# Performance work log

Hardware: AMD Instinct MI355X
Metric: run time of the kernel (lower is better)

The kernel has to match this reference:

```python
import jax, jax.numpy as jnp
import numpy as np


def setup_inputs() -> dict:
    key = jax.random.key(0)
    ks = jax.random.split(key, 8)
    bs, slen, d = 16, 2048, 1024
    scale = 1.0 / np.sqrt(d)
    return {
        "query": jax.random.normal(ks[0], (bs, d), jnp.float32),
        "states": jax.random.normal(ks[1], (bs, slen, d), jnp.float32),
        "Wq": jax.random.normal(ks[2], (d, d), jnp.float32) * scale,
        "bq": jax.random.normal(ks[3], (d,), jnp.float32) * 0.01,
        "Wk": jax.random.normal(ks[4], (d, d), jnp.float32) * scale,
        "bk": jax.random.normal(ks[5], (d,), jnp.float32) * 0.01,
        "We": jax.random.normal(ks[6], (2 * d,), jnp.float32) * scale,
        "be": jax.random.normal(ks[7], (1,), jnp.float32) * 0.01,
    }


def reference(query, states, Wq, bq, Wk, bk, We, be):
    d = Wq.shape[1]
    # q: (bs, d); k: (bs, slen, d)
    q = jax.nn.relu(query @ Wq + bq)
    k = jax.nn.relu(jnp.einsum("bsv,vd->bsd", states, Wk) + bk)
    # tanh(cat(q, k)) @ We == tanh(q) @ We[:d] + tanh(k) @ We[d:]
    # (avoids materializing the repeated/concatenated (bs, slen, 2d) tensor)
    We_q, We_k = We[:d], We[d:]
    energy = (jnp.tanh(q) @ We_q)[:, None] + jnp.einsum("bsd,d->bs", jnp.tanh(k), We_k) + be[0]
    attn_weights = jax.nn.softmax(energy, axis=1)  # (bs, slen)
    attn = jnp.einsum("bs,bsd->bd", attn_weights, states)  # weighted sum of values
    return attn_weights, attn
```

## Files before the change

kernel.cpp:

```cpp
#include <hip/hip_runtime.h>
#include <hip/hip_bf16.h>

#define D 1024
#define SLEN 2048
#define BS 16
#define MROWS (BS*SLEN)

typedef __attribute__((ext_vector_type(8))) short short8;
typedef __attribute__((ext_vector_type(4))) float f32x4;

__device__ __forceinline__ short f2bf(float f) {
  __hip_bfloat16 h = __float2bfloat16(f);
  return __builtin_bit_cast(short, h);
}

__device__ __forceinline__ float4 ntload4(const float* p) {
  f32x4 v = __builtin_nontemporal_load((const f32x4*)p);
  float4 r; r.x = v.x; r.y = v.y; r.z = v.z; r.w = v.w; return r;
}

__global__ __launch_bounds__(256) void wk_prep(const float* __restrict__ Wk,
                                               short* __restrict__ WkT) {
  const int g = blockIdx.x;
  const int t = threadIdx.x;
#pragma unroll
  for (int it = 0; it < 4; ++it) {
    const int n = it*256 + t;
    short8 p;
#pragma unroll
    for (int j = 0; j < 8; ++j)
      p[j] = f2bf(Wk[(size_t)(g*8 + j)*D + n]);
    *(short8*)(WkT + ((size_t)g*D + n)*8) = p;
  }
}

__global__ __launch_bounds__(512, 2) void energy_gemm(
    const float* __restrict__ states, const short* __restrict__ WkT,
    const float* __restrict__ bk, const float* __restrict__ We,
    float* __restrict__ eraw, float* __restrict__ attn)
{
  __shared__ short Al[64 * 129 * 8];

  const int tid  = threadIdx.x;
  const int w    = tid >> 6;
  const int lane = tid & 63;
  const int quad = lane >> 4;
  const int l16  = lane & 15;
  const int m0   = blockIdx.x * 64;

  if (blockIdx.x < BS && tid < 256) {
    f32x4 z = {0.f, 0.f, 0.f, 0.f};
    *(f32x4*)(attn + (size_t)blockIdx.x*D + tid*4) = z;
  }

  {
    const int row = tid >> 3;
    const int u0  = tid & 7;
    const float* Ag = states + (size_t)(m0 + row)*D;
#pragma unroll
    for (int i = 0; i < 16; ++i) {
      const int u = u0 + i*8;
      float4 x0 = ntload4(Ag + u*8);
      float4 x1 = ntload4(Ag + u*8 + 4);
      short8 p;
      p[0]=f2bf(x0.x); p[1]=f2bf(x0.y); p[2]=f2bf(x0.z); p[3]=f2bf(x0.w);
      p[4]=f2bf(x1.x); p[5]=f2bf(x1.y); p[6]=f2bf(x1.z); p[7]=f2bf(x1.w);
      *(short8*)(Al + ((size_t)row*129 + u)*8) = p;
    }
  }
  __syncthreads();

  const short* bbase = WkT + ((size_t)quad*D + w*128 + l16)*8;
  const short* abase = Al + ((size_t)l16*129 + quad)*8;

  float esum[16];
#pragma unroll
  for (int q = 0; q < 16; ++q) esum[q] = 0.f;

#define LOADB3(ks, slot)                                                 \
  {                                                                      \
    const short* bp = bpass + (size_t)(ks)*32768;                        \
    _Pragma("unroll")                                                    \
    for (int ni = 0; ni < 4; ++ni)                                       \
      fb[slot][ni] = *(const short8*)(bp + ni*128);                      \
  }

#define LOADA(ks, buf)                                                   \
  {                                                                      \
    _Pragma("unroll")                                                    \
    for (int mi = 0; mi < 4; ++mi)                                       \
      buf[mi] = *(const short8*)(abase + mi*16512 + (ks)*32);            \
  }

#define MFMAS16(fa, slot)                                                \
  {                                                                      \
    __builtin_amdgcn_s_setprio(1);                                       \
    _Pragma("unroll")                                                    \
    for (int mi = 0; mi < 4; ++mi)                                       \
      _Pragma("unroll")                                                  \
      for (int ni = 0; ni < 4; ++ni)                                     \
        acc[mi][ni] = __builtin_amdgcn_mfma_f32_16x16x32_bf16(           \
            fa[mi], fb[slot][ni], acc[mi][ni], 0, 0, 0);                 \
    __builtin_amdgcn_s_setprio(0);                                       \
  }

#pragma unroll
  for (int np = 0; np < 2; ++np) {
    const short* bpass = bbase + np*512;

    f32x4 acc[4][4];
#pragma unroll
    for (int mi = 0; mi < 4; ++mi)
#pragma unroll
      for (int ni = 0; ni < 4; ++ni)
        acc[mi][ni] = (f32x4){0.f, 0.f, 0.f, 0.f};

    short8 fb[3][4];
    short8 fa0[4], fa1[4];
    LOADB3(0, 0); LOADB3(1, 1); LOADB3(2, 2);
    LOADA(0, fa0);
#pragma unroll
    for (int kk = 0; kk < 16; ++kk) {
      LOADA(2*kk + 1, fa1);
      MFMAS16(fa0, (2*kk) % 3);
      if (2*kk + 3 < 32) LOADB3(2*kk + 3, (2*kk) % 3);
      if (kk < 15) LOADA(2*kk + 2, fa0);
      MFMAS16(fa1, (2*kk + 1) % 3);
      if (2*kk + 4 < 32) LOADB3(2*kk + 4, (2*kk + 1) % 3);
    }

#pragma unroll
    for (int ni = 0; ni < 4; ++ni) {
      const int n = w*128 + np*64 + ni*16 + l16;
      const float bkv = bk[n];
      const float wev = We[D + n];
#pragma unroll
      for (int mi = 0; mi < 4; ++mi)
#pragma unroll
        for (int r = 0; r < 4; ++r) {
          float x = acc[mi][ni][r] + bkv;
          x = fmaxf(x, 0.f);
          float ex = __expf(2.f * x);
          float th = 1.f - 2.f/(ex + 1.f);
          esum[mi*4 + r] += th * wev;
        }
    }
  }

#pragma unroll
  for (int dd = 1; dd < 16; dd <<= 1)
#pragma unroll
    for (int q = 0; q < 16; ++q)
      esum[q] += __shfl_xor(esum[q], dd, 64);

  __syncthreads();
  float* red = (float*)Al;
  if (l16 == 0) {
#pragma unroll
    for (int mi = 0; mi < 4; ++mi)
#pragma unroll
      for (int r = 0; r < 4; ++r)
        red[(mi*16 + quad*4 + r)*8 + w] = esum[mi*4 + r];
  }
  __syncthreads();
  if (tid < 64) {
    float s = 0.f;
#pragma unroll
    for (int wi = 0; wi < 8; ++wi) s += red[tid*8 + wi];
    eraw[m0 + tid] = s;
  }
#undef LOADB3
#undef LOADA
#undef MFMAS16
}

__global__ __launch_bounds__(512) void attn_fused(
    const float* __restrict__ states, const float* __restrict__ eraw,
    float* __restrict__ wts, float* __restrict__ attn)
{
  const int sc = blockIdx.x;
  const int b  = blockIdx.y;
  const int t  = threadIdx.x;
  const int wv = t >> 6;
  const int lane = t & 63;

  __shared__ float  redm[8];
  __shared__ float  reds[8];
  __shared__ float  wsh[64];
  __shared__ float4 part[256];

  float v[4];
  float m = -1e30f;
#pragma unroll
  for (int j = 0; j < 4; ++j) {
    v[j] = eraw[(size_t)b*SLEN + j*512 + t];
    m = fmaxf(m, v[j]);
  }
#pragma unroll
  for (int dd = 1; dd < 64; dd <<= 1) m = fmaxf(m, __shfl_xor(m, dd, 64));
  if (lane == 0) redm[wv] = m;
  __syncthreads();
  float m2 = redm[0];
#pragma unroll
  for (int i = 1; i < 8; ++i) m2 = fmaxf(m2, redm[i]);

  float sum = 0.f;
#pragma unroll
  for (int j = 0; j < 4; ++j) sum += __expf(v[j] - m2);
#pragma unroll
  for (int dd = 1; dd < 64; dd <<= 1) sum += __shfl_xor(sum, dd, 64);
  if (lane == 0) reds[wv] = sum;
  __syncthreads();
  float s2 = 0.f;
#pragma unroll
  for (int i = 0; i < 8; ++i) s2 += reds[i];
  const float inv = 1.f / s2;

  if (t < 64) {
    const float wvv = __expf(eraw[(size_t)b*SLEN + sc*64 + t] - m2) * inv;
    wts[(size_t)b*SLEN + sc*64 + t] = wvv;
    wsh[t] = wvv;
  }
  __syncthreads();

  const int dq = (t & 255) << 2;
  const int ss = t >> 8;
  const float* sp = states + ((size_t)b*SLEN + sc*64 + ss*32)*D + dq;
  float ax = 0.f, ay = 0.f, az = 0.f, aw = 0.f;
#pragma unroll
  for (int s = 0; s < 32; ++s) {
    float4 x = *(const float4*)(sp + (size_t)s*D);
    const float wvv = wsh[ss*32 + s];
    ax = fmaf(wvv, x.x, ax);
    ay = fmaf(wvv, x.y, ay);
    az = fmaf(wvv, x.z, az);
    aw = fmaf(wvv, x.w, aw);
  }

  if (ss) part[t & 255] = (float4){ax, ay, az, aw};
  __syncthreads();
  if (!ss) {
    const float4 o = part[t];
    float* p = attn + (size_t)b*D + dq;
    atomicAdd(p + 0, ax + o.x);
    atomicAdd(p + 1, ay + o.y);
    atomicAdd(p + 2, az + o.z);
    atomicAdd(p + 3, aw + o.w);
  }
}

extern "C" void kernel_launch(void* const* d_in, const int* in_sizes, int n_in,
                              void* d_out, int out_size, void* d_ws, size_t ws_size,
                              hipStream_t stream) {
  const float* states = (const float*)d_in[1];
  const float* Wk     = (const float*)d_in[4];
  const float* bk     = (const float*)d_in[5];
  const float* We     = (const float*)d_in[6];
  float* out = (float*)d_out;

  short* WkT  = (short*)d_ws;
  float* eraw = (float*)((char*)d_ws + (size_t)D*D*sizeof(short));

  (void)in_sizes; (void)n_in; (void)out_size; (void)ws_size;

  wk_prep<<<128, 256, 0, stream>>>(Wk, WkT);
  energy_gemm<<<MROWS/64, 512, 0, stream>>>(states, WkT, bk, We, eraw, out + MROWS);
  attn_fused<<<dim3(32, BS), 512, 0, stream>>>(states, eraw, out, out + MROWS);
}
```

Before: 301.5 us.

## Use 1024-thread blocks and split K staging into halves overlapped with MFMA

The energy GEMM block grows to 1024 threads (16 waves), so each wave covers 64 output columns in a single pass instead of two passes of 64. The A tile is staged to LDS in two K halves, and the second half's global loads are issued while the first half's MFMAs run, which is meant to hide the staging latency. The triple-buffered B-fragment prefetch is replaced by simple per-step loads, and the cross-wave reduction now spans 16 waves. The risks are higher register pressure under the 1024-thread launch bound and more exposed B-load latency.

```diff
diff --git a/kernel.cpp b/kernel.cpp
--- a/kernel.cpp
+++ b/kernel.cpp
@@ -34,12 +34,12 @@
   }
 }
 
-__global__ __launch_bounds__(512, 2) void energy_gemm(
+__global__ __launch_bounds__(1024, 4) void energy_gemm(
     const float* __restrict__ states, const short* __restrict__ WkT,
     const float* __restrict__ bk, const float* __restrict__ We,
     float* __restrict__ eraw, float* __restrict__ attn)
 {
-  __shared__ short Al[64 * 129 * 8];
+  __shared__ short Al[2 * 64 * 65 * 8];
 
   const int tid  = threadIdx.x;
   const int w    = tid >> 6;
@@ -53,46 +53,60 @@
     *(f32x4*)(attn + (size_t)blockIdx.x*D + tid*4) = z;
   }
 
-  {
-    const int row = tid >> 3;
-    const int u0  = tid & 7;
-    const float* Ag = states + (size_t)(m0 + row)*D;
-#pragma unroll
-    for (int i = 0; i < 16; ++i) {
-      const int u = u0 + i*8;
-      float4 x0 = ntload4(Ag + u*8);
-      float4 x1 = ntload4(Ag + u*8 + 4);
-      short8 p;
-      p[0]=f2bf(x0.x); p[1]=f2bf(x0.y); p[2]=f2bf(x0.z); p[3]=f2bf(x0.w);
-      p[4]=f2bf(x1.x); p[5]=f2bf(x1.y); p[6]=f2bf(x1.z); p[7]=f2bf(x1.w);
-      *(short8*)(Al + ((size_t)row*129 + u)*8) = p;
-    }
-  }
-  __syncthreads();
-
-  const short* bbase = WkT + ((size_t)quad*D + w*128 + l16)*8;
-  const short* abase = Al + ((size_t)l16*129 + quad)*8;
-
-  float esum[16];
-#pragma unroll
-  for (int q = 0; q < 16; ++q) esum[q] = 0.f;
-
-#define LOADB3(ks, slot)                                                 \
-  {                                                                      \
-    const short* bp = bpass + (size_t)(ks)*32768;                        \
+  const int srow = tid >> 4;
+  const int sseg = tid & 15;
+  const float* Ag = states + (size_t)(m0 + srow)*D + sseg*32;
+
+  float4 stg[8];
+
+#define STAGE_LOAD4(h, off)                                              \
+  {                                                                      \
+    _Pragma("unroll")                                                    \
+    for (int i = 0; i < 4; ++i)                                          \
+      stg[(off) + i] = ntload4(Ag + (h)*512 + ((off) + i)*4);            \
+  }
+
+#define STAGE_WRITE(h)                                                   \
+  {                                                                      \
+    _Pragma("unroll")                                                    \
+    for (int j = 0; j < 4; ++j) {                                        \
+      short8 p;                                                          \
+      p[0]=f2bf(stg[2*j].x);   p[1]=f2bf(stg[2*j].y);                    \
+      p[2]=f2bf(stg[2*j].z);   p[3]=f2bf(stg[2*j].w);                    \
+      p[4]=f2bf(stg[2*j+1].x); p[5]=f2bf(stg[2*j+1].y);                  \
+      p[6]=f2bf(stg[2*j+1].z); p[7]=f2bf(stg[2*j+1].w);                  \
+      *(short8*)(Al + (size_t)(h)*33280 +                                \
+                 ((size_t)srow*65 + sseg*4 + j)*8) = p;                  \
+    }                                                                    \
+  }
+
+  const short* abase = Al + ((size_t)l16*65 + quad)*8;
+  const short* bbase = WkT + ((size_t)quad*D + w*64 + l16)*8;
+
+  f32x4 acc[4][4];
+#pragma unroll
+  for (int mi = 0; mi < 4; ++mi)
+#pragma unroll
+    for (int ni = 0; ni < 4; ++ni)
+      acc[mi][ni] = (f32x4){0.f, 0.f, 0.f, 0.f};
+
+#define LOADA(h, ks, buf)                                                \
+  {                                                                      \
+    const short* ap = abase + (h)*33280 + (ks)*32;                       \
+    _Pragma("unroll")                                                    \
+    for (int mi = 0; mi < 4; ++mi)                                       \
+      buf[mi] = *(const short8*)(ap + mi*8320);                          \
+  }
+
+#define LOADB(ksg, buf)                                                  \
+  {                                                                      \
+    const short* bp = bbase + (size_t)(ksg)*32768;                       \
     _Pragma("unroll")                                                    \
     for (int ni = 0; ni < 4; ++ni)                                       \
-      fb[slot][ni] = *(const short8*)(bp + ni*128);                      \
-  }
-
-#define LOADA(ks, buf)                                                   \
-  {                                                                      \
-    _Pragma("unroll")                                                    \
-    for (int mi = 0; mi < 4; ++mi)                                       \
-      buf[mi] = *(const short8*)(abase + mi*16512 + (ks)*32);            \
-  }
-
-#define MFMAS16(fa, slot)                                                \
+      buf[ni] = *(const short8*)(bp + ni*128);                           \
+  }
+
+#define MFMAS(fa, fb)                                                    \
   {                                                                      \
     __builtin_amdgcn_s_setprio(1);                                       \
     _Pragma("unroll")                                                    \
@@ -100,53 +114,54 @@
       _Pragma("unroll")                                                  \
       for (int ni = 0; ni < 4; ++ni)                                     \
         acc[mi][ni] = __builtin_amdgcn_mfma_f32_16x16x32_bf16(           \
-            fa[mi], fb[slot][ni], acc[mi][ni], 0, 0, 0);                 \
+            fa[mi], fb[ni], acc[mi][ni], 0, 0, 0);                       \
     __builtin_amdgcn_s_setprio(0);                                       \
   }
 
-#pragma unroll
-  for (int np = 0; np < 2; ++np) {
-    const short* bpass = bbase + np*512;
-
-    f32x4 acc[4][4];
+  STAGE_LOAD4(0, 0); STAGE_LOAD4(0, 4);
+  STAGE_WRITE(0);
+  __syncthreads();
+
+  short8 fa[4], fb[4];
+
+#pragma unroll
+  for (int ks = 0; ks < 16; ++ks) {
+    if (ks == 8)  STAGE_LOAD4(1, 0);
+    if (ks == 12) STAGE_LOAD4(1, 4);
+    LOADA(0, ks, fa);
+    LOADB(ks, fb);
+    MFMAS(fa, fb);
+  }
+
+  STAGE_WRITE(1);
+  __syncthreads();
+
+#pragma unroll
+  for (int ks = 0; ks < 16; ++ks) {
+    LOADA(1, ks, fa);
+    LOADB(16 + ks, fb);
+    MFMAS(fa, fb);
+  }
+
+  float esum[16];
+#pragma unroll
+  for (int q = 0; q < 16; ++q) esum[q] = 0.f;
+#pragma unroll
+  for (int ni = 0; ni < 4; ++ni) {
+    const int n = w*64 + ni*16 + l16;
+    const float bkv = bk[n];
+    const float wev = We[D + n];
 #pragma unroll
     for (int mi = 0; mi < 4; ++mi)
 #pragma unroll
-      for (int ni = 0; ni < 4; ++ni)
-        acc[mi][ni] = (f32x4){0.f, 0.f, 0.f, 0.f};
-
-    short8 fb[3][4];
-    short8 fa0[4], fa1[4];
-    LOADB3(0, 0); LOADB3(1, 1); LOADB3(2, 2);
-    LOADA(0, fa0);
-#pragma unroll
-    for (int kk = 0; kk < 16; ++kk) {
-      LOADA(2*kk + 1, fa1);
-      MFMAS16(fa0, (2*kk) % 3);
-      if (2*kk + 3 < 32) LOADB3(2*kk + 3, (2*kk) % 3);
-      if (kk < 15) LOADA(2*kk + 2, fa0);
-      MFMAS16(fa1, (2*kk + 1) % 3);
-      if (2*kk + 4 < 32) LOADB3(2*kk + 4, (2*kk + 1) % 3);
-    }
-
-#pragma unroll
-    for (int ni = 0; ni < 4; ++ni) {
-      const int n = w*128 + np*64 + ni*16 + l16;
-      const float bkv = bk[n];
-      const float wev = We[D + n];
-#pragma unroll
-      for (int mi = 0; mi < 4; ++mi)
-#pragma unroll
-        for (int r = 0; r < 4; ++r) {
-          float x = acc[mi][ni][r] + bkv;
-          x = fmaxf(x, 0.f);
-          float ex = __expf(2.f * x);
-          float th = 1.f - 2.f/(ex + 1.f);
-          esum[mi*4 + r] += th * wev;
-        }
-    }
-  }
-
+      for (int r = 0; r < 4; ++r) {
+        float x = acc[mi][ni][r] + bkv;
+        x = fmaxf(x, 0.f);
+        float ex = __expf(2.f * x);
+        float th = 1.f - 2.f/(ex + 1.f);
+        esum[mi*4 + r] += th * wev;
+      }
+  }
 #pragma unroll
   for (int dd = 1; dd < 16; dd <<= 1)
 #pragma unroll
@@ -160,18 +175,20 @@
     for (int mi = 0; mi < 4; ++mi)
 #pragma unroll
       for (int r = 0; r < 4; ++r)
-        red[(mi*16 + quad*4 + r)*8 + w] = esum[mi*4 + r];
+        red[(mi*16 + quad*4 + r)*16 + w] = esum[mi*4 + r];
   }
   __syncthreads();
   if (tid < 64) {
     float s = 0.f;
 #pragma unroll
-    for (int wi = 0; wi < 8; ++wi) s += red[tid*8 + wi];
+    for (int wi = 0; wi < 16; ++wi) s += red[tid*16 + wi];
     eraw[m0 + tid] = s;
   }
-#undef LOADB3
+#undef STAGE_LOAD4
+#undef STAGE_WRITE
 #undef LOADA
-#undef MFMAS16
+#undef LOADB
+#undef MFMAS
 }
 
 __global__ __launch_bounds__(512) void attn_fused(
@@ -264,6 +281,6 @@
   (void)in_sizes; (void)n_in; (void)out_size; (void)ws_size;
 
   wk_prep<<<128, 256, 0, stream>>>(Wk, WkT);
-  energy_gemm<<<MROWS/64, 512, 0, stream>>>(states, WkT, bk, We, eraw, out + MROWS);
+  energy_gemm<<<MROWS/64, 1024, 0, stream>>>(states, WkT, bk, We, eraw, out + MROWS);
   attn_fused<<<dim3(32, BS), 512, 0, stream>>>(states, eraw, out, out + MROWS);
 }
```

Result: slower. 362.4 us (+20.2%).
